# Performance work log

Measured on AMD Instinct MI355X. Metric: run time of the kernel, lower is better.

The kernel has to match this reference:

```python
import jax, jax.numpy as jnp
import numpy as np

WINDOW = 16
STRIDE = 8
PADDING = 0
EPS = 1e-6


def setup_inputs() -> dict:
    key = jax.random.key(0)
    x = jax.random.normal(key, (4, 32, 256, 256), dtype=jnp.float32)
    return {"x": x}


def reference(x):
    # Faithful translation of ExtractTensorPatches.forward:
    # grouped conv2d with an (identity + eps) one-hot kernel per channel,
    # so out_i = patch_elem_i + eps * sum(patch).
    B, C, H, W = x.shape
    w2 = WINDOW * WINDOW
    # (w2, 1, w, w): diag = 1+eps, off-diag = eps (matches create_kernel)
    k = (jnp.eye(w2, dtype=x.dtype) + jnp.asarray(EPS, x.dtype)).reshape(
        w2, 1, WINDOW, WINDOW
    )
    k = jnp.tile(k, (C, 1, 1, 1))  # (C*w2, 1, w, w), group-major like torch repeat
    out = jax.lax.conv_general_dilated(
        x,
        k,
        window_strides=(STRIDE, STRIDE),
        padding=[(PADDING, PADDING), (PADDING, PADDING)],
        feature_group_count=C,
        dimension_numbers=("NCHW", "OIHW", "NCHW"),
    )  # (B, C*w2, Ho, Wo)
    Ho, Wo = out.shape[2], out.shape[3]
    out = out.reshape(B, C, WINDOW, WINDOW, Ho * Wo)
    return jnp.transpose(out, (0, 4, 1, 2, 3))  # (B, L, C, w, w)
```

## Files before the change

### kernel.cpp

```cpp
#include <hip/hip_runtime.h>


#define BB   4
#define CC   32
#define HH   256
#define WW   256
#define STR  8
#define HOC  31
#define WOC  31
#define LL   (HOC * WOC)
#define EPSF 1e-6f
#define PITCH 272

__global__ __launch_bounds__(256) void
extract_patches_strip(const float* __restrict__ x, float* __restrict__ out) {
    __shared__ float strip[16 * PITCH];
    __shared__ float cs[16 * 32];
    __shared__ float epsP[32];

    const int tid = threadIdx.x;
    const int c   = blockIdx.x;
    const int ho  = blockIdx.y;
    const int b   = blockIdx.z;

    const float* src = x + ((size_t)(b * CC + c) * HH + (size_t)(ho * STR)) * WW;

#pragma unroll
    for (int it = 0; it < 4; ++it) {
        const int g   = (it * 256 + tid) * 4;
        const float4 v = *(const float4*)(src + g);
        const int row = g >> 8;
        const int col = g & 255;
        *(float4*)(&strip[row * PITCH + col]) = v;
        float s4 = v.x + v.y + v.z + v.w;
        s4 += __shfl_xor(s4, 1, 64);
        if ((tid & 1) == 0)
            cs[g >> 3] = s4;
    }
    __syncthreads();

    if (tid < WOC) {
        float s = 0.f;
#pragma unroll
        for (int r = 0; r < 16; ++r)
            s += cs[r * 32 + 2 * tid] + cs[r * 32 + 2 * tid + 1];
        epsP[tid] = EPSF * s;
    }
    __syncthreads();

    const int wave  = tid >> 6;
    const int lane  = tid & 63;
    const int prow  = lane >> 2;
    const int pcol4 = (lane & 3) * 4;
    float* dstbase = out
        + (((size_t)b * LL + (size_t)ho * WOC) * CC + c) * 256
        + (size_t)(lane * 4);
#pragma unroll
    for (int p = 0; p < 8; ++p) {
        const int wo = p * 4 + wave;
        if (wo < WOC) {
            const float4 v =
                *(const float4*)(&strip[prow * PITCH + wo * STR + pcol4]);
            const float e = epsP[wo];
            const float4 o = make_float4(v.x + e, v.y + e, v.z + e, v.w + e);
            *(float4*)(dstbase + ((size_t)wo << 13)) = o;
        }
    }
}

extern "C" void kernel_launch(void* const* d_in, const int* in_sizes, int n_in,
                              void* d_out, int out_size, void* d_ws, size_t ws_size,
                              hipStream_t stream) {
    const float* x = (const float*)d_in[0];
    float* out = (float*)d_out;

    dim3 grid(CC, HOC, BB);
    dim3 block(256);
    extract_patches_strip<<<grid, block, 0, stream>>>(x, out);
}
```

Measured before the change: 149.1 us.

## Compute each patch per wave directly from global memory with XCD-swizzled blocks

Replaces the shared-memory strip kernel with a flat kernel in which each wave loads one 16x16 patch straight from global memory and reduces its sum with wave shuffles. Each block covers four channels of a single output location, so the four waves write 4KB of contiguous output. Block IDs are remapped so consecutive work lands on the same XCD, and output is written with nontemporal stores. This drops LDS traffic and barriers, but each input element is now read about four times instead of once (windows overlap), relying on L2 to absorb the repeats, and many more tiny blocks are launched.

Measured after the change: 170.5 us. 1.14x slower.

```diff
diff --git a/kernel.cpp b/kernel.cpp
--- a/kernel.cpp
+++ b/kernel.cpp
@@ -10,62 +10,47 @@
 #define WOC  31
 #define LL   (HOC * WOC)
 #define EPSF 1e-6f
-#define PITCH 272
+#define NXCD 8
+#define CGRP 4
+#define NGY  (CC / CGRP)
+
+typedef float f4 __attribute__((ext_vector_type(4)));
 
 __global__ __launch_bounds__(256) void
-extract_patches_strip(const float* __restrict__ x, float* __restrict__ out) {
-    __shared__ float strip[16 * PITCH];
-    __shared__ float cs[16 * 32];
-    __shared__ float epsP[32];
+extract_patches_flat(const float* __restrict__ x, float* __restrict__ out) {
+    const int nwg  = LL * NGY * BB;
+    const int cpx  = nwg / NXCD;
+    const int hwid = blockIdx.x + LL * (blockIdx.y + NGY * blockIdx.z);
+    const int swz  = (hwid % NXCD) * cpx + (hwid / NXCD);
 
-    const int tid = threadIdx.x;
-    const int c   = blockIdx.x;
-    const int ho  = blockIdx.y;
-    const int b   = blockIdx.z;
+    const int l    = swz % LL;
+    const int rest = swz / LL;
+    const int gy   = rest & (NGY - 1);
+    const int b    = rest >> 3;
 
-    const float* src = x + ((size_t)(b * CC + c) * HH + (size_t)(ho * STR)) * WW;
+    const int wave = threadIdx.x >> 6;
+    const int lane = threadIdx.x & 63;
+    const int c    = gy * CGRP + wave;
 
+    const int ho = l / WOC;
+    const int wo = l - ho * WOC;
+    const int r  = lane >> 2;
+    const int q  = lane & 3;
+
+    const float* px = x
+        + (((size_t)(b * CC + c) * HH + (size_t)(ho * STR + r)) * WW
+           + (size_t)(wo * STR + q * 4));
+    const f4 v = *(const f4*)px;
+
+    float s = v.x + v.y + v.z + v.w;
 #pragma unroll
-    for (int it = 0; it < 4; ++it) {
-        const int g   = (it * 256 + tid) * 4;
-        const float4 v = *(const float4*)(src + g);
-        const int row = g >> 8;
-        const int col = g & 255;
-        *(float4*)(&strip[row * PITCH + col]) = v;
-        float s4 = v.x + v.y + v.z + v.w;
-        s4 += __shfl_xor(s4, 1, 64);
-        if ((tid & 1) == 0)
-            cs[g >> 3] = s4;
-    }
-    __syncthreads();
+    for (int d = 1; d < 64; d <<= 1)
+        s += __shfl_xor(s, d, 64);
 
-    if (tid < WOC) {
-        float s = 0.f;
-#pragma unroll
-        for (int r = 0; r < 16; ++r)
-            s += cs[r * 32 + 2 * tid] + cs[r * 32 + 2 * tid + 1];
-        epsP[tid] = EPSF * s;
-    }
-    __syncthreads();
+    const f4 o = v + (EPSF * s);
 
-    const int wave  = tid >> 6;
-    const int lane  = tid & 63;
-    const int prow  = lane >> 2;
-    const int pcol4 = (lane & 3) * 4;
-    float* dstbase = out
-        + (((size_t)b * LL + (size_t)ho * WOC) * CC + c) * 256
-        + (size_t)(lane * 4);
-#pragma unroll
-    for (int p = 0; p < 8; ++p) {
-        const int wo = p * 4 + wave;
-        if (wo < WOC) {
-            const float4 v =
-                *(const float4*)(&strip[prow * PITCH + wo * STR + pcol4]);
-            const float e = epsP[wo];
-            const float4 o = make_float4(v.x + e, v.y + e, v.z + e, v.w + e);
-            *(float4*)(dstbase + ((size_t)wo << 13)) = o;
-        }
-    }
+    float* po = out + (((size_t)b * LL + l) * CC + c) * 256 + (size_t)(lane * 4);
+    __builtin_nontemporal_store(o, (f4*)po);
 }
 
 extern "C" void kernel_launch(void* const* d_in, const int* in_sizes, int n_in,
@@ -74,7 +59,7 @@
     const float* x = (const float*)d_in[0];
     float* out = (float*)d_out;
 
-    dim3 grid(CC, HOC, BB);
+    dim3 grid(LL, NGY, BB);
     dim3 block(256);
-    extract_patches_strip<<<grid, block, 0, stream>>>(x, out);
+    extract_patches_flat<<<grid, block, 0, stream>>>(x, out);
 }
```

## Split patch extraction into sum pass and per-patch emit kernel with nontemporal stores

Applied to the files above, without the earlier changes.

Adds a first kernel that computes each patch's eps-scaled sum into workspace, and a second kernel that emits one full output patch (all channels) per block, so each block writes one contiguous 32KB region. Output stores in both paths now use nontemporal stores, meant to cut cache pollution from the large write stream. The emit kernel reads input with overlapping 64-byte row segments across 32 channel planes, which may be less efficient than the original strip staging. There is an extra launch, and the original fused kernel is kept as a fallback when workspace is missing. The column-sum indexing is also corrected to use adjacent 8-wide chunks.

Result: slower. 180.7 us (+21.2%).

```diff
diff --git a/kernel.cpp b/kernel.cpp
--- a/kernel.cpp
+++ b/kernel.cpp
@@ -10,28 +10,22 @@
 #define WOC  31
 #define LL   (HOC * WOC)
 #define EPSF 1e-6f
-#define PITCH 272
+
+typedef float f4 __attribute__((ext_vector_type(4)));
 
 __global__ __launch_bounds__(256) void
-extract_patches_strip(const float* __restrict__ x, float* __restrict__ out) {
-    __shared__ float strip[16 * PITCH];
+patch_sums(const float* __restrict__ x, float* __restrict__ psum) {
     __shared__ float cs[16 * 32];
-    __shared__ float epsP[32];
-
     const int tid = threadIdx.x;
     const int c   = blockIdx.x;
     const int ho  = blockIdx.y;
     const int b   = blockIdx.z;
-
     const float* src = x + ((size_t)(b * CC + c) * HH + (size_t)(ho * STR)) * WW;
 
 #pragma unroll
     for (int it = 0; it < 4; ++it) {
-        const int g   = (it * 256 + tid) * 4;
-        const float4 v = *(const float4*)(src + g);
-        const int row = g >> 8;
-        const int col = g & 255;
-        *(float4*)(&strip[row * PITCH + col]) = v;
+        const int g = (it * 256 + tid) * 4;
+        const f4 v  = *(const f4*)(src + g);
         float s4 = v.x + v.y + v.z + v.w;
         s4 += __shfl_xor(s4, 1, 64);
         if ((tid & 1) == 0)
@@ -43,27 +37,82 @@
         float s = 0.f;
 #pragma unroll
         for (int r = 0; r < 16; ++r)
-            s += cs[r * 32 + 2 * tid] + cs[r * 32 + 2 * tid + 1];
+            s += cs[r * 32 + tid] + cs[r * 32 + tid + 1];
+        psum[((size_t)b * LL + (size_t)ho * WOC + tid) * CC + c] = s;
+    }
+}
+
+__global__ __launch_bounds__(256) void
+emit_patches(const float* __restrict__ x, const float* __restrict__ psum,
+             float* __restrict__ out) {
+    __shared__ float eps_s[CC];
+    const int tid = threadIdx.x;
+    const int l   = blockIdx.x;
+    const int b   = blockIdx.y;
+    const int ho  = l / WOC;
+    const int wo  = l - ho * WOC;
+
+    if (tid < CC)
+        eps_s[tid] = EPSF * psum[((size_t)b * LL + l) * CC + tid];
+    __syncthreads();
+
+    const int q4 = tid & 63;
+    const int r  = q4 >> 2;
+    const int qc = (q4 & 3) * 4;
+    const int w0 = tid >> 6;
+
+    const float* xb = x + ((size_t)(b * CC) * HH + (size_t)(ho * STR + r)) * WW
+                        + (size_t)(wo * STR + qc);
+    float* ob = out + ((size_t)b * LL + l) * (CC * 256) + (size_t)(tid * 4);
+
+#pragma unroll
+    for (int k = 0; k < 8; ++k) {
+        const int c = k * 4 + w0;
+        const f4 v  = *(const f4*)(xb + (size_t)c * (HH * WW));
+        const f4 o  = v + eps_s[c];
+        __builtin_nontemporal_store(o, (f4*)(ob + k * 1024));
+    }
+}
+
+#define PITCH 272
+__global__ __launch_bounds__(256) void
+extract_patches_strip(const float* __restrict__ x, float* __restrict__ out) {
+    __shared__ float strip[16 * PITCH];
+    __shared__ float cs[16 * 32];
+    __shared__ float epsP[32];
+    const int tid = threadIdx.x;
+    const int c = blockIdx.x, ho = blockIdx.y, b = blockIdx.z;
+    const float* src = x + ((size_t)(b * CC + c) * HH + (size_t)(ho * STR)) * WW;
+#pragma unroll
+    for (int it = 0; it < 4; ++it) {
+        const int g = (it * 256 + tid) * 4;
+        const f4 v = *(const f4*)(src + g);
+        const int row = g >> 8, col = g & 255;
+        *(f4*)(&strip[row * PITCH + col]) = v;
+        float s4 = v.x + v.y + v.z + v.w;
+        s4 += __shfl_xor(s4, 1, 64);
+        if ((tid & 1) == 0) cs[g >> 3] = s4;
+    }
+    __syncthreads();
+    if (tid < WOC) {
+        float s = 0.f;
+#pragma unroll
+        for (int r = 0; r < 16; ++r)
+            s += cs[r * 32 + tid] + cs[r * 32 + tid + 1];
         epsP[tid] = EPSF * s;
     }
     __syncthreads();
-
-    const int wave  = tid >> 6;
-    const int lane  = tid & 63;
-    const int prow  = lane >> 2;
-    const int pcol4 = (lane & 3) * 4;
-    float* dstbase = out
-        + (((size_t)b * LL + (size_t)ho * WOC) * CC + c) * 256
-        + (size_t)(lane * 4);
+    const int wave = tid >> 6, lane = tid & 63;
+    const int prow = lane >> 2, pcol4 = (lane & 3) * 4;
+    float* dstbase = out + (((size_t)b * LL + (size_t)ho * WOC) * CC + c) * 256
+                   + (size_t)(lane * 4);
 #pragma unroll
     for (int p = 0; p < 8; ++p) {
         const int wo = p * 4 + wave;
         if (wo < WOC) {
-            const float4 v =
-                *(const float4*)(&strip[prow * PITCH + wo * STR + pcol4]);
+            const f4 v = *(const f4*)(&strip[prow * PITCH + wo * STR + pcol4]);
             const float e = epsP[wo];
-            const float4 o = make_float4(v.x + e, v.y + e, v.z + e, v.w + e);
-            *(float4*)(dstbase + ((size_t)wo << 13)) = o;
+            __builtin_nontemporal_store(v + e, (f4*)(dstbase + ((size_t)wo << 13)));
         }
     }
 }
@@ -73,8 +122,13 @@
                               hipStream_t stream) {
     const float* x = (const float*)d_in[0];
     float* out = (float*)d_out;
+    const size_t psum_bytes = (size_t)BB * LL * CC * sizeof(float);
 
-    dim3 grid(CC, HOC, BB);
-    dim3 block(256);
-    extract_patches_strip<<<grid, block, 0, stream>>>(x, out);
+    if (ws_size >= psum_bytes && d_ws != nullptr) {
+        float* psum = (float*)d_ws;
+        patch_sums<<<dim3(CC, HOC, BB), dim3(256), 0, stream>>>(x, psum);
+        emit_patches<<<dim3(LL, BB), dim3(256), 0, stream>>>(x, psum, out);
+    } else {
+        extract_patches_strip<<<dim3(CC, HOC, BB), dim3(256), 0, stream>>>(x, out);
+    }
 }
```
